# Kernel tuning notes

Measured on AMD Instinct MI355X. Metric: run time of the kernel, lower is better.

## Reference

```python
import jax, jax.numpy as jnp
import numpy as np

# Hardcoded in FixedActionDecoder.__init__:
# action_words = [[click,submit,target,focus],[select,text,noun,username,password],[copy],[paste]]
ACTION_INDEX = jnp.array([0, 0, 0, 0, 1, 1, 1, 1, 1, 2, 3], dtype=jnp.int32)
POINT_SIZE = 11
ACTION_SIZE = 4
EPS = 1e-8  # F.cosine_similarity default eps


def setup_inputs() -> dict:
    key = jax.random.key(0)
    k1, k2 = jax.random.split(key)
    B, D = 1_000_000, 64
    return {
        "embedded_words": jax.random.normal(k1, (B, D), dtype=jnp.float32),
        "action_vectors": jax.random.normal(k2, (D, POINT_SIZE), dtype=jnp.float32),
    }


def reference(embedded_words, action_vectors):
    # Cosine similarity along the embedding dim (torch clamps each norm to eps).
    x = embedded_words / jnp.maximum(
        jnp.linalg.norm(embedded_words, axis=1, keepdims=True), EPS)          # [B, D]
    a = action_vectors / jnp.maximum(
        jnp.linalg.norm(action_vectors, axis=0, keepdims=True), EPS)          # [D, P]
    sims = x @ a                                                              # [B, P]
    # global_max_pool over batch_action_index == per-batch segment-max over actions.
    seg = jax.ops.segment_max(sims.T, ACTION_INDEX,
                              num_segments=ACTION_SIZE).T                     # [B, A]
    action_idx = jnp.argmax(seg, axis=1)                                      # [B]
    # one-hot scatter: ret[action_idx] = 1.0
    return jax.nn.one_hot(action_idx, ACTION_SIZE, dtype=embedded_words.dtype)
```

## Files before the change

### kernel.cpp

```cpp
#include <hip/hip_runtime.h>


#define NP 11
#define TAU 1e-3f
#define LROW 36

__device__ __align__(16) float g_W32[704];
__device__ double g_W64[704];
__device__ unsigned long long g_bits[1 << 20];

__global__ void prep(const float* __restrict__ A) {
    __shared__ double sq[64][NP + 1];
    __shared__ double sc[NP];
    const int d = threadIdx.x;
    double a[NP];
    #pragma unroll
    for (int p = 0; p < NP; ++p) {
        a[p] = (double)A[d * NP + p];
        sq[d][p] = a[p] * a[p];
    }
    __syncthreads();
    if (d < NP) {
        double ss = 0.0;
        #pragma unroll
        for (int r = 0; r < 64; ++r) ss += sq[r][d];
        sc[d] = 1.0 / fmax(sqrt(ss), 1e-8);
    }
    __syncthreads();
    #pragma unroll
    for (int p = 0; p < NP; ++p) {
        double w = a[p] * sc[p];
        g_W64[d * NP + p] = w;
        g_W32[(d >> 2) * 44 + p * 4 + (d & 3)] = (float)w;
    }
}

__device__ __forceinline__ void argmax_gap(const float* s, int& idx, float& gap) {
    float m0 = fmaxf(fmaxf(s[0], s[1]), fmaxf(s[2], s[3]));
    float m1 = fmaxf(fmaxf(fmaxf(s[4], s[5]), s[6]), fmaxf(s[7], s[8]));
    float m2 = s[9], m3 = s[10];
    idx = 0; float best = m0;
    if (m1 > best) { best = m1; idx = 1; }
    if (m2 > best) { best = m2; idx = 2; }
    if (m3 > best) { best = m3; idx = 3; }
    float second = -3.4e38f;
    if (idx != 0) second = fmaxf(second, m0);
    if (idx != 1) second = fmaxf(second, m1);
    if (idx != 2) second = fmaxf(second, m2);
    if (idx != 3) second = fmaxf(second, m3);
    gap = best - second;
}

__global__ __launch_bounds__(128) void decode(const float* __restrict__ X,
                                              float* __restrict__ out, int B) {
    __shared__ float xbuf[2][128][LROW];
    __shared__ float w_lds[704];

    const int tid = threadIdx.x;
    const int lane = tid & 63;
    const int wv = tid >> 6;
    float(*buf)[LROW] = xbuf[wv];

    for (int t = tid; t < 176; t += 128)
        reinterpret_cast<float4*>(w_lds)[t] =
            reinterpret_cast<const float4*>(g_W32)[t];
    __syncthreads();

    const float4* X4 = reinterpret_cast<const float4*>(X);
    const int gwave = blockIdx.x * 2 + wv;
    const int nwaves = gridDim.x * 2;

    #pragma unroll 1
    for (int base = gwave * 128; base < B; base += nwaves * 128) {
        float acc0[NP], acc1[NP];
        #pragma unroll
        for (int p = 0; p < NP; ++p) { acc0[p] = 0.0f; acc1[p] = 0.0f; }

        #pragma unroll
        for (int st = 0; st < 2; ++st) {
            #pragma unroll
            for (int i = 0; i < 16; ++i) {
                int fid = i * 64 + lane;
                int row = fid >> 3;
                int f = fid & 7;
                int r = base + row;
                if (r >= B) r = B - 1;
                float4 v = X4[(size_t)r * 16 + st * 8 + f];
                *reinterpret_cast<float4*>(&buf[row][f * 4]) = v;
            }
            __builtin_amdgcn_wave_barrier();

            #pragma unroll 1
            for (int kk = 0; kk < 8; ++kk) {
                const float* wrow = &w_lds[(st * 8 + kk) * 44];
                float4 x0 = *reinterpret_cast<const float4*>(&buf[lane][kk * 4]);
                float4 x1 = *reinterpret_cast<const float4*>(&buf[lane + 64][kk * 4]);
                #pragma unroll
                for (int p = 0; p < NP; ++p) {
                    float4 wq = *reinterpret_cast<const float4*>(&wrow[p * 4]);
                    float t0 = fmaf(x0.x, wq.x, acc0[p]);
                    t0 = fmaf(x0.y, wq.y, t0);
                    t0 = fmaf(x0.z, wq.z, t0);
                    acc0[p] = fmaf(x0.w, wq.w, t0);
                    float t1 = fmaf(x1.x, wq.x, acc1[p]);
                    t1 = fmaf(x1.y, wq.y, t1);
                    t1 = fmaf(x1.z, wq.z, t1);
                    acc1[p] = fmaf(x1.w, wq.w, t1);
                }
            }
            __builtin_amdgcn_wave_barrier();
        }

        int idx0, idx1; float gap0, gap1;
        argmax_gap(acc0, idx0, gap0);
        argmax_gap(acc1, idx1, gap1);

        unsigned long long m0 = __ballot(gap0 < TAU);
        unsigned long long m1 = __ballot(gap1 < TAU);
        if (lane == 0) {
            g_bits[(base >> 6) + 0] = m0;
            g_bits[(base >> 6) + 1] = m1;
        }

        int r0 = base + lane, r1 = base + 64 + lane;
        if (r0 < B) {
            float4 o;
            o.x = (idx0 == 0) ? 1.0f : 0.0f;
            o.y = (idx0 == 1) ? 1.0f : 0.0f;
            o.z = (idx0 == 2) ? 1.0f : 0.0f;
            o.w = (idx0 == 3) ? 1.0f : 0.0f;
            reinterpret_cast<float4*>(out)[r0] = o;
        }
        if (r1 < B) {
            float4 o;
            o.x = (idx1 == 0) ? 1.0f : 0.0f;
            o.y = (idx1 == 1) ? 1.0f : 0.0f;
            o.z = (idx1 == 2) ? 1.0f : 0.0f;
            o.w = (idx1 == 3) ? 1.0f : 0.0f;
            reinterpret_cast<float4*>(out)[r1] = o;
        }
    }
}

__global__ __launch_bounds__(256) void repair(const float* __restrict__ X,
                                              float* __restrict__ out, int B) {
    __shared__ double w64[704];
    const int tid = threadIdx.x;
    for (int i = tid; i < 704; i += 256) w64[i] = g_W64[i];
    __syncthreads();

    const int nwords = (B + 63) >> 6;
    for (int t = blockIdx.x * blockDim.x + tid; t < nwords;
         t += gridDim.x * blockDim.x) {
        unsigned long long m = g_bits[t];
        while (m) {
            int b = __builtin_ctzll(m);
            m &= m - 1;
            int row = t * 64 + b;
            if (row >= B) continue;

            double s[NP];
            #pragma unroll
            for (int p = 0; p < NP; ++p) s[p] = 0.0;
            #pragma unroll 1
            for (int d = 0; d < 64; ++d) {
                double x = (double)X[(size_t)row * 64 + d];
                #pragma unroll
                for (int p = 0; p < NP; ++p)
                    s[p] = fma(x, w64[d * NP + p], s[p]);
            }

            double m0 = fmax(fmax(s[0], s[1]), fmax(s[2], s[3]));
            double m1 = fmax(fmax(fmax(s[4], s[5]), s[6]), fmax(s[7], s[8]));
            double m2 = s[9], m3 = s[10];
            int idx = 0; double best = m0;
            if (m1 > best) { best = m1; idx = 1; }
            if (m2 > best) { best = m2; idx = 2; }
            if (m3 > best) { best = m3; idx = 3; }

            float4 o;
            o.x = (idx == 0) ? 1.0f : 0.0f;
            o.y = (idx == 1) ? 1.0f : 0.0f;
            o.z = (idx == 2) ? 1.0f : 0.0f;
            o.w = (idx == 3) ? 1.0f : 0.0f;
            reinterpret_cast<float4*>(out)[row] = o;
        }
    }
}

extern "C" void kernel_launch(void* const* d_in, const int* in_sizes, int n_in,
                              void* d_out, int out_size, void* d_ws, size_t ws_size,
                              hipStream_t stream) {
    const float* X = (const float*)d_in[0];
    const float* A = (const float*)d_in[1];
    float* out = (float*)d_out;
    const int B = in_sizes[0] / 64;

    hipLaunchKernelGGL(prep, dim3(1), dim3(64), 0, stream, A);
    hipLaunchKernelGGL(decode, dim3(1024), dim3(128), 0, stream, X, out, B);
    hipLaunchKernelGGL(repair, dim3(128), dim3(256), 0, stream, X, out, B);
}
```

Before: 78.28 us.

## Software-pipeline global loads into registers while computing the previous LDS half-tile

Restructures the decode loop so each wave issues the global loads for the next half-tile into sixteen float4 registers, then runs the dot-product compute on the half-tile already in LDS before committing the new data. The first half of the next tile is prefetched while the second half of the current tile is computed. The goal is to hide global memory latency behind FMA work in this bandwidth-bound kernel, at the cost of 64 extra VGPRs per thread, which may reduce occupancy. Sched barriers stop the compiler from moving the loads past the compute.

```diff
diff --git a/kernel.cpp b/kernel.cpp
--- a/kernel.cpp
+++ b/kernel.cpp
@@ -51,6 +51,45 @@
     gap = best - second;
 }
 
+#define LOADN(n, tb, ph)                                                       \
+    {                                                                          \
+        int rr = (tb) + (n)*8 + hi3;                                           \
+        if (rr >= B) rr = B - 1;            \
+        pf##n = X4[(size_t)rr * 16 + (ph)*8 + f8];                             \
+    }
+#define ISSUE(tb, ph)                                                          \
+    LOADN(0, tb, ph) LOADN(1, tb, ph) LOADN(2, tb, ph) LOADN(3, tb, ph)        \
+    LOADN(4, tb, ph) LOADN(5, tb, ph) LOADN(6, tb, ph) LOADN(7, tb, ph)        \
+    LOADN(8, tb, ph) LOADN(9, tb, ph) LOADN(10, tb, ph) LOADN(11, tb, ph)      \
+    LOADN(12, tb, ph) LOADN(13, tb, ph) LOADN(14, tb, ph) LOADN(15, tb, ph)
+
+#define COMMN(n) *reinterpret_cast<float4*>(&buf[(n)*8 + hi3][f8 * 4]) = pf##n;
+#define COMMIT()                                                               \
+    COMMN(0) COMMN(1) COMMN(2) COMMN(3) COMMN(4) COMMN(5) COMMN(6) COMMN(7)    \
+    COMMN(8) COMMN(9) COMMN(10) COMMN(11) COMMN(12) COMMN(13) COMMN(14)        \
+    COMMN(15)
+
+#define COMPUTE(ph)                                                            \
+    {                                                                          \
+        _Pragma("unroll 1") for (int kk = 0; kk < 8; ++kk) {                   \
+            const float* wrow = &w_lds[((ph)*8 + kk) * 44];                    \
+            float4 x0 = *reinterpret_cast<const float4*>(&buf[lane][kk * 4]);  \
+            float4 x1 =                                                        \
+                *reinterpret_cast<const float4*>(&buf[lane + 64][kk * 4]);     \
+            _Pragma("unroll") for (int p = 0; p < NP; ++p) {                   \
+                float4 wq = *reinterpret_cast<const float4*>(&wrow[p * 4]);    \
+                float t0 = fmaf(x0.x, wq.x, acc0[p]);                          \
+                t0 = fmaf(x0.y, wq.y, t0);                                     \
+                t0 = fmaf(x0.z, wq.z, t0);                                     \
+                acc0[p] = fmaf(x0.w, wq.w, t0);                                \
+                float t1 = fmaf(x1.x, wq.x, acc1[p]);                          \
+                t1 = fmaf(x1.y, wq.y, t1);                                     \
+                t1 = fmaf(x1.z, wq.z, t1);                                     \
+                acc1[p] = fmaf(x1.w, wq.w, t1);                                \
+            }                                                                  \
+        }                                                                      \
+    }
+
 __global__ __launch_bounds__(128) void decode(const float* __restrict__ X,
                                               float* __restrict__ out, int B) {
     __shared__ float xbuf[2][128][LROW];
@@ -67,49 +106,40 @@
     __syncthreads();
 
     const float4* X4 = reinterpret_cast<const float4*>(X);
+    const int f8 = lane & 7;
+    const int hi3 = lane >> 3;
     const int gwave = blockIdx.x * 2 + wv;
     const int nwaves = gridDim.x * 2;
+    const int stride = nwaves * 128;
+    const int base0 = gwave * 128;
+    if (base0 >= B) return;
+
+    float4 pf0, pf1, pf2, pf3, pf4, pf5, pf6, pf7;
+    float4 pf8, pf9, pf10, pf11, pf12, pf13, pf14, pf15;
+
+    ISSUE(base0, 0)
+    COMMIT()
+    __builtin_amdgcn_wave_barrier();
 
     #pragma unroll 1
-    for (int base = gwave * 128; base < B; base += nwaves * 128) {
+    for (int base = base0; base < B; base += stride) {
+        int nb = base + stride;
+        if (nb >= B) nb = base;
+
         float acc0[NP], acc1[NP];
         #pragma unroll
         for (int p = 0; p < NP; ++p) { acc0[p] = 0.0f; acc1[p] = 0.0f; }
 
-        #pragma unroll
-        for (int st = 0; st < 2; ++st) {
-            #pragma unroll
-            for (int i = 0; i < 16; ++i) {
-                int fid = i * 64 + lane;
-                int row = fid >> 3;
-                int f = fid & 7;
-                int r = base + row;
-                if (r >= B) r = B - 1;
-                float4 v = X4[(size_t)r * 16 + st * 8 + f];
-                *reinterpret_cast<float4*>(&buf[row][f * 4]) = v;
-            }
-            __builtin_amdgcn_wave_barrier();
-
-            #pragma unroll 1
-            for (int kk = 0; kk < 8; ++kk) {
-                const float* wrow = &w_lds[(st * 8 + kk) * 44];
-                float4 x0 = *reinterpret_cast<const float4*>(&buf[lane][kk * 4]);
-                float4 x1 = *reinterpret_cast<const float4*>(&buf[lane + 64][kk * 4]);
-                #pragma unroll
-                for (int p = 0; p < NP; ++p) {
-                    float4 wq = *reinterpret_cast<const float4*>(&wrow[p * 4]);
-                    float t0 = fmaf(x0.x, wq.x, acc0[p]);
-                    t0 = fmaf(x0.y, wq.y, t0);
-                    t0 = fmaf(x0.z, wq.z, t0);
-                    acc0[p] = fmaf(x0.w, wq.w, t0);
-                    float t1 = fmaf(x1.x, wq.x, acc1[p]);
-                    t1 = fmaf(x1.y, wq.y, t1);
-                    t1 = fmaf(x1.z, wq.z, t1);
-                    acc1[p] = fmaf(x1.w, wq.w, t1);
-                }
-            }
-            __builtin_amdgcn_wave_barrier();
-        }
+        ISSUE(base, 1)
+        __builtin_amdgcn_sched_barrier(0);
+        COMPUTE(0)
+        __builtin_amdgcn_wave_barrier();
+        COMMIT()
+        __builtin_amdgcn_wave_barrier();
+
+        ISSUE(nb, 0)
+        __builtin_amdgcn_sched_barrier(0);
+        COMPUTE(1)
 
         int idx0, idx1; float gap0, gap1;
         argmax_gap(acc0, idx0, gap0);
@@ -139,6 +169,10 @@
             o.w = (idx1 == 3) ? 1.0f : 0.0f;
             reinterpret_cast<float4*>(out)[r1] = o;
         }
+
+        __builtin_amdgcn_wave_barrier();
+        COMMIT()
+        __builtin_amdgcn_wave_barrier();
     }
 }
 
```

Result: slower. 83.44 us (+6.6%).
